# Kernel tuning notes

Hardware: AMD Instinct MI355X
Metric: run time of the kernel (lower is better)

Reference implementation:

```python
import jax, jax.numpy as jnp
import numpy as np

EPS = 1e-7
BETA = 1.0


def setup_inputs() -> dict:
    key = jax.random.key(0)
    k1, k2, k3, k4 = jax.random.split(key, 4)
    N, E, D_IN, D_OUT = 50000, 800000, 96, 96
    feat = jax.random.normal(k1, (N, D_IN), dtype=jnp.float32)
    src = jax.random.randint(k2, (E,), 0, N, dtype=jnp.int32)
    dst = jax.random.randint(k3, (E,), 0, N, dtype=jnp.int32)
    W = jax.random.normal(k4, (D_IN, D_OUT), dtype=jnp.float32) / np.sqrt(D_IN)
    b = jnp.zeros((D_OUT,), dtype=jnp.float32)
    return {"feat": feat, "src": src, "dst": dst, "W": W, "b": b}


def reference(feat, src, dst, W, b):
    # GENConv with softmax aggregation (canonical DeeperGCN semantics):
    # per edge e=(u,v): m_e = relu(h_u) + eps
    #                   a_e = softmax over edges into v of (beta * m_e)  (per feature dim)
    #                   msg_v = sum_e a_e * m_e
    # out = MLP(h + msg), MLP here = single Linear (mlp_layers=1)
    N = feat.shape[0]
    m = jax.nn.relu(feat[src]) + EPS                     # [E, D]
    logits = BETA * m                                    # [E, D]
    # numerically stable segment softmax over incoming edges of each dst node
    seg_max = jax.ops.segment_max(logits, dst, num_segments=N)   # [N, D]
    ex = jnp.exp(logits - seg_max[dst])                  # [E, D]
    denom = jax.ops.segment_sum(ex, dst, num_segments=N)         # [N, D]
    a = ex / denom[dst]                                  # [E, D]
    msg = jax.ops.segment_sum(a * m, dst, num_segments=N)        # [N, D]
    feats = feat + msg                                   # residual
    return feats @ W + b                                 # [N, D_out]
```

## Files before the change

### kernel.cpp

```cpp
#include <hip/hip_runtime.h>

#define D 96
#define EPSV 1e-7f
#define STRIDE 64
#define NB 16
#define TFUSED 192
#define EPB 2048
#define CAP 5120
#define HLP 100

__device__ __forceinline__ unsigned short f32_to_bf16_rtne(float x) {
    unsigned int u = __float_as_uint(x);
    u += 0x7fffu + ((u >> 16) & 1u);
    return (unsigned short)(u >> 16);
}
__device__ __forceinline__ float blo(uint u) { return __uint_as_float(u << 16); }
__device__ __forceinline__ float bhi(uint u) { return __uint_as_float(u & 0xFFFF0000u); }
__device__ __forceinline__ float bf16_to_f32(unsigned short u) {
    return __uint_as_float(((unsigned int)u) << 16);
}

__global__ __launch_bounds__(256) void part_conv(
    const int* __restrict__ src, const int* __restrict__ dst,
    uint* __restrict__ cursor,
    uint* __restrict__ stage,
    int E, int pblk,
    const float* __restrict__ feat, ushort* __restrict__ fb, int total4)
{
    __shared__ uint   hist[256];
    __shared__ uint   scn[256];
    __shared__ uint   xbase[256];
    __shared__ uint   gbase[256];
    __shared__ uint   sorted[EPB];
    __shared__ ushort sbid[EPB];

    int t = threadIdx.x;

    if ((int)blockIdx.x >= pblk) {
        int i = ((int)blockIdx.x - pblk) * 256 + t;
        if (i < total4) {
            const float4 f = reinterpret_cast<const float4*>(feat)[i];
            ushort4 o;
            o.x = f32_to_bf16_rtne(f.x);
            o.y = f32_to_bf16_rtne(f.y);
            o.z = f32_to_bf16_rtne(f.z);
            o.w = f32_to_bf16_rtne(f.w);
            reinterpret_cast<ushort4*>(fb)[i] = o;
        }
        return;
    }

    int e0 = blockIdx.x * EPB;
    int tot = E - e0; if (tot > EPB) tot = EPB;

    hist[t] = 0;
    __syncthreads();

    uint myb[EPB / 256], myrk[EPB / 256], myrec[EPB / 256];
    #pragma unroll
    for (int r = 0; r < EPB / 256; ++r) {
        int i = r * 256 + t;
        if (i < tot) {
            int d = dst[e0 + i];
            int s = src[e0 + i];
            uint b = (uint)d >> 8;
            myb[r]  = b;
            myrk[r] = atomicAdd(&hist[b], 1u);
            myrec[r] = (uint)(s & 0xFFFF) | ((uint)(d & 0xFF) << 16);
        }
    }
    __syncthreads();

    scn[t] = hist[t];
    __syncthreads();
    #pragma unroll
    for (int off = 1; off < 256; off <<= 1) {
        uint v = (t >= off) ? scn[t - off] : 0u;
        __syncthreads();
        scn[t] += v;
        __syncthreads();
    }
    xbase[t] = scn[t] - hist[t];
    if (hist[t] > 0)
        gbase[t] = (uint)t * CAP + atomicAdd(&cursor[t], hist[t]);
    __syncthreads();

    #pragma unroll
    for (int r = 0; r < EPB / 256; ++r) {
        int i = r * 256 + t;
        if (i < tot) {
            uint j = xbase[myb[r]] + myrk[r];
            sorted[j] = myrec[r];
            sbid[j]   = (ushort)myb[r];
        }
    }
    __syncthreads();

    #pragma unroll
    for (int r = 0; r < EPB / 256; ++r) {
        int j = r * 256 + t;
        if (j < tot) {
            uint b = sbid[j];
            uint gaddr = gbase[b] + ((uint)j - xbase[b]);
            if (gaddr - b * CAP < CAP)
                stage[gaddr] = sorted[j];
        }
    }
}

__global__ __launch_bounds__(256) void csr_build(
    const uint* __restrict__ cursor, const uint* __restrict__ stage,
    int* __restrict__ deg, ushort* __restrict__ csr, int N)
{
    __shared__ int ldeg[256];
    int b = blockIdx.x;
    int t = threadIdx.x;
    ldeg[t] = 0;
    __syncthreads();

    int cnt = (int)cursor[b]; if (cnt > CAP) cnt = CAP;
    const uint* sp = stage + (size_t)b * CAP;
    for (int i = t; i < cnt; i += 256) {
        uint rec = sp[i];
        int s  = rec & 0xFFFF;
        int dl = (rec >> 16) & 0xFF;
        int slot = atomicAdd(&ldeg[dl], 1);
        if (slot < STRIDE)
            csr[(size_t)((b << 8) + dl) * STRIDE + slot] = (ushort)s;
    }
    __syncthreads();
    int n = (b << 8) + t;
    if (n < N) deg[n] = min(ldeg[t], STRIDE);
}

__global__ __launch_bounds__(256) void build_fast(
    const float* __restrict__ feat, ushort* __restrict__ fb, int total4,
    const int* __restrict__ src, const int* __restrict__ dst,
    int* __restrict__ deg, ushort* __restrict__ csr, int E)
{
    int i = blockIdx.x * 256 + threadIdx.x;
    if (i < total4) {
        const float4 f = reinterpret_cast<const float4*>(feat)[i];
        ushort4 o;
        o.x = f32_to_bf16_rtne(f.x);
        o.y = f32_to_bf16_rtne(f.y);
        o.z = f32_to_bf16_rtne(f.z);
        o.w = f32_to_bf16_rtne(f.w);
        reinterpret_cast<ushort4*>(fb)[i] = o;
    } else {
        int e = i - total4;
        if (e < E) {
            int d = dst[e];
            int pos = atomicAdd(&deg[d], 1);
            if (pos < STRIDE) csr[(size_t)d * STRIDE + pos] = (ushort)src[e];
        }
    }
}

__global__ __launch_bounds__(TFUSED, 4) void fused_gather_gemm(
    const float* __restrict__ feat,
    const ushort* __restrict__ fb,
    const int* __restrict__ degp,
    const ushort* __restrict__ csr,
    const float* __restrict__ W,
    const float* __restrict__ bias,
    float* __restrict__ out,
    int N)
{
    __shared__ float  hl[NB][HLP];
    __shared__ ushort csr_l[NB * STRIDE];
    __shared__ int    degl[NB];

    int t = threadIdx.x;
    int nb0 = blockIdx.x * NB;

    {
        int nodes = N - nb0; if (nodes > NB) nodes = NB;
        int avail4 = (nodes * STRIDE) / 8;
        const uint4* gsrc = reinterpret_cast<const uint4*>(csr + (size_t)nb0 * STRIDE);
        uint4* ldst = reinterpret_cast<uint4*>(csr_l);
        if (t < avail4) ldst[t] = gsrc[t];
        if (t >= 128 && t < 128 + NB) {
            int nl = t - 128;
            int n = nb0 + nl;
            degl[nl] = (n < N) ? min(degp[n], STRIDE) : 0;
        }
    }
    __syncthreads();

    {
        int nl = t / 12;
        int q  = (t % 12) * 8;
        int n  = nb0 + nl;
        if (n < N) {
            int c = degl[nl];
            const ushort* cl = &csr_l[nl * STRIDE];

            float d0=0.f,d1=0.f,d2=0.f,d3=0.f,d4=0.f,d5=0.f,d6=0.f,d7=0.f;
            float a0=0.f,a1=0.f,a2=0.f,a3=0.f,a4=0.f,a5=0.f,a6=0.f,a7=0.f;

            #define PROC8(U) { \
                float m0 = fmaxf(blo((U).x), 0.f) + EPSV; \
                float m1 = fmaxf(bhi((U).x), 0.f) + EPSV; \
                float m2 = fmaxf(blo((U).y), 0.f) + EPSV; \
                float m3 = fmaxf(bhi((U).y), 0.f) + EPSV; \
                float m4 = fmaxf(blo((U).z), 0.f) + EPSV; \
                float m5 = fmaxf(bhi((U).z), 0.f) + EPSV; \
                float m6 = fmaxf(blo((U).w), 0.f) + EPSV; \
                float m7 = fmaxf(bhi((U).w), 0.f) + EPSV; \
                float e0=__expf(m0), e1=__expf(m1), e2=__expf(m2), e3=__expf(m3); \
                float e4=__expf(m4), e5=__expf(m5), e6=__expf(m6), e7=__expf(m7); \
                d0+=e0; d1+=e1; d2+=e2; d3+=e3; d4+=e4; d5+=e5; d6+=e6; d7+=e7; \
                a0=fmaf(e0,m0,a0); a1=fmaf(e1,m1,a1); a2=fmaf(e2,m2,a2); a3=fmaf(e3,m3,a3); \
                a4=fmaf(e4,m4,a4); a5=fmaf(e5,m5,a5); a6=fmaf(e6,m6,a6); a7=fmaf(e7,m7,a7); }

            int j = 0;
            for (; j + 4 <= c; j += 4) {
                const ushort4 ia = *reinterpret_cast<const ushort4*>(cl + j);
                const uint4 u0 = *reinterpret_cast<const uint4*>(fb + (size_t)ia.x * D + q);
                const uint4 u1 = *reinterpret_cast<const uint4*>(fb + (size_t)ia.y * D + q);
                const uint4 u2 = *reinterpret_cast<const uint4*>(fb + (size_t)ia.z * D + q);
                const uint4 u3 = *reinterpret_cast<const uint4*>(fb + (size_t)ia.w * D + q);
                PROC8(u0); PROC8(u1); PROC8(u2); PROC8(u3);
            }
            for (; j < c; ++j) {
                int s = cl[j];
                const uint4 u = *reinterpret_cast<const uint4*>(fb + (size_t)s * D + q);
                PROC8(u);
            }
            #undef PROC8

            const float4 bA = *reinterpret_cast<const float4*>(feat + (size_t)n * D + q);
            const float4 bB = *reinterpret_cast<const float4*>(feat + (size_t)n * D + q + 4);
            bool has = c > 0;
            float4 hA, hB;
            hA.x = bA.x + (has ? a0 / d0 : 0.f);
            hA.y = bA.y + (has ? a1 / d1 : 0.f);
            hA.z = bA.z + (has ? a2 / d2 : 0.f);
            hA.w = bA.w + (has ? a3 / d3 : 0.f);
            hB.x = bB.x + (has ? a4 / d4 : 0.f);
            hB.y = bB.y + (has ? a5 / d5 : 0.f);
            hB.z = bB.z + (has ? a6 / d6 : 0.f);
            hB.w = bB.w + (has ? a7 / d7 : 0.f);
            *reinterpret_cast<float4*>(&hl[nl][q])     = hA;
            *reinterpret_cast<float4*>(&hl[nl][q + 4]) = hB;
        }
    }
    __syncthreads();

    int q   = (t % 24) * 4;
    int grp = t / 24;
    int r0 = grp * 2, r1 = r0 + 1;
    float4 acc0 = *reinterpret_cast<const float4*>(bias + q);
    float4 acc1 = acc0;

    #pragma unroll 4
    for (int k = 0; k < D; ++k) {
        const float4 w = *reinterpret_cast<const float4*>(W + k * D + q);
        float h0 = hl[r0][k];
        float h1 = hl[r1][k];
        acc0.x = fmaf(h0, w.x, acc0.x); acc0.y = fmaf(h0, w.y, acc0.y);
        acc0.z = fmaf(h0, w.z, acc0.z); acc0.w = fmaf(h0, w.w, acc0.w);
        acc1.x = fmaf(h1, w.x, acc1.x); acc1.y = fmaf(h1, w.y, acc1.y);
        acc1.z = fmaf(h1, w.z, acc1.z); acc1.w = fmaf(h1, w.w, acc1.w);
    }

    int n0 = nb0 + r0;
    if (n0 + 0 < N) *reinterpret_cast<float4*>(out + (size_t)(n0 + 0) * D + q) = acc0;
    if (n0 + 1 < N) *reinterpret_cast<float4*>(out + (size_t)(n0 + 1) * D + q) = acc1;
}

extern "C" void kernel_launch(void* const* d_in, const int* in_sizes, int n_in,
                              void* d_out, int out_size, void* d_ws, size_t ws_size,
                              hipStream_t stream) {
    const float* feat = (const float*)d_in[0];
    const int*   src  = (const int*)d_in[1];
    const int*   dst  = (const int*)d_in[2];
    const float* W    = (const float*)d_in[3];
    const float* bias = (const float*)d_in[4];

    int N = in_sizes[0] / D;
    int E = in_sizes[1];
    int total4 = N * D / 4;
    int nbuck  = (N + 255) >> 8;

    size_t fb_bytes    = (size_t)N * D * sizeof(ushort);
    size_t deg_bytes   = (size_t)N * sizeof(int);
    size_t csr_bytes   = (size_t)N * STRIDE * sizeof(ushort);
    size_t cur_bytes   = 256 * sizeof(uint);
    size_t stage_bytes = (size_t)nbuck * CAP * sizeof(uint);

    size_t part_need  = fb_bytes + deg_bytes + csr_bytes + cur_bytes + stage_bytes;
    size_t fast_need  = fb_bytes + deg_bytes + csr_bytes;

    int gblocks = (N + NB - 1) / NB;

    ushort* fb  = (ushort*)d_ws;
    int*    deg = (int*)((char*)d_ws + fb_bytes);
    ushort* csr = (ushort*)((char*)deg + deg_bytes);

    if (ws_size >= part_need) {
        uint* cursor = (uint*)((char*)csr + csr_bytes);
        uint* stage  = (uint*)((char*)cursor + cur_bytes);

        int pblk = (E + EPB - 1) / EPB;
        int cblk = (total4 + 255) / 256;

        (void)hipMemsetAsync(cursor, 0, cur_bytes, stream);
        part_conv<<<pblk + cblk, 256, 0, stream>>>(
            src, dst, cursor, stage, E, pblk, feat, fb, total4);
        csr_build<<<nbuck, 256, 0, stream>>>(cursor, stage, deg, csr, N);
        fused_gather_gemm<<<gblocks, TFUSED, 0, stream>>>(
            feat, fb, deg, csr, W, bias, (float*)d_out, N);
    } else if (ws_size >= fast_need) {
        (void)hipMemsetAsync(deg, 0, deg_bytes, stream);
        int btotal = total4 + E;
        build_fast<<<(btotal + 255) / 256, 256, 0, stream>>>(
            feat, fb, total4, src, dst, deg, csr, E);
        fused_gather_gemm<<<gblocks, TFUSED, 0, stream>>>(
            feat, fb, deg, csr, W, bias, (float*)d_out, N);
    }
}
```

Before: 84.93 us.

## Scatter edges directly to global buckets and unroll gather loop by eight

The partition kernel no longer runs a block-wide prefix scan and local shared-memory sort before writing to the staging buckets. Each edge now goes straight to its global bucket slot, computed from the bucket base plus its atomic rank. This removes the scan's many syncs and the shared-memory traffic, but the global writes become less coalesced. Separately, the aggregation loop processes eight neighbor rows per iteration instead of four, putting more gathers in flight at the cost of more registers.

Result: slower. 92.01 us (+8.3%).

```diff
diff --git a/kernel.cpp b/kernel.cpp
--- a/kernel.cpp
+++ b/kernel.cpp
@@ -16,9 +16,6 @@
 }
 __device__ __forceinline__ float blo(uint u) { return __uint_as_float(u << 16); }
 __device__ __forceinline__ float bhi(uint u) { return __uint_as_float(u & 0xFFFF0000u); }
-__device__ __forceinline__ float bf16_to_f32(unsigned short u) {
-    return __uint_as_float(((unsigned int)u) << 16);
-}
 
 __global__ __launch_bounds__(256) void part_conv(
     const int* __restrict__ src, const int* __restrict__ dst,
@@ -27,12 +24,8 @@
     int E, int pblk,
     const float* __restrict__ feat, ushort* __restrict__ fb, int total4)
 {
-    __shared__ uint   hist[256];
-    __shared__ uint   scn[256];
-    __shared__ uint   xbase[256];
-    __shared__ uint   gbase[256];
-    __shared__ uint   sorted[EPB];
-    __shared__ ushort sbid[EPB];
+    __shared__ uint hist[256];
+    __shared__ uint gbase[256];
 
     int t = threadIdx.x;
 
@@ -71,16 +64,6 @@
     }
     __syncthreads();
 
-    scn[t] = hist[t];
-    __syncthreads();
-    #pragma unroll
-    for (int off = 1; off < 256; off <<= 1) {
-        uint v = (t >= off) ? scn[t - off] : 0u;
-        __syncthreads();
-        scn[t] += v;
-        __syncthreads();
-    }
-    xbase[t] = scn[t] - hist[t];
     if (hist[t] > 0)
         gbase[t] = (uint)t * CAP + atomicAdd(&cursor[t], hist[t]);
     __syncthreads();
@@ -89,21 +72,10 @@
     for (int r = 0; r < EPB / 256; ++r) {
         int i = r * 256 + t;
         if (i < tot) {
-            uint j = xbase[myb[r]] + myrk[r];
-            sorted[j] = myrec[r];
-            sbid[j]   = (ushort)myb[r];
-        }
-    }
-    __syncthreads();
-
-    #pragma unroll
-    for (int r = 0; r < EPB / 256; ++r) {
-        int j = r * 256 + t;
-        if (j < tot) {
-            uint b = sbid[j];
-            uint gaddr = gbase[b] + ((uint)j - xbase[b]);
+            uint b = myb[r];
+            uint gaddr = gbase[b] + myrk[r];
             if (gaddr - b * CAP < CAP)
-                stage[gaddr] = sorted[j];
+                stage[gaddr] = myrec[r];
         }
     }
 }
@@ -215,13 +187,28 @@
                 a4=fmaf(e4,m4,a4); a5=fmaf(e5,m5,a5); a6=fmaf(e6,m6,a6); a7=fmaf(e7,m7,a7); }
 
             int j = 0;
-            for (; j + 4 <= c; j += 4) {
+            for (; j + 8 <= c; j += 8) {
+                const ushort4 ia = *reinterpret_cast<const ushort4*>(cl + j);
+                const ushort4 ib = *reinterpret_cast<const ushort4*>(cl + j + 4);
+                const uint4 u0 = *reinterpret_cast<const uint4*>(fb + (size_t)ia.x * D + q);
+                const uint4 u1 = *reinterpret_cast<const uint4*>(fb + (size_t)ia.y * D + q);
+                const uint4 u2 = *reinterpret_cast<const uint4*>(fb + (size_t)ia.z * D + q);
+                const uint4 u3 = *reinterpret_cast<const uint4*>(fb + (size_t)ia.w * D + q);
+                const uint4 u4 = *reinterpret_cast<const uint4*>(fb + (size_t)ib.x * D + q);
+                const uint4 u5 = *reinterpret_cast<const uint4*>(fb + (size_t)ib.y * D + q);
+                const uint4 u6 = *reinterpret_cast<const uint4*>(fb + (size_t)ib.z * D + q);
+                const uint4 u7 = *reinterpret_cast<const uint4*>(fb + (size_t)ib.w * D + q);
+                PROC8(u0); PROC8(u1); PROC8(u2); PROC8(u3);
+                PROC8(u4); PROC8(u5); PROC8(u6); PROC8(u7);
+            }
+            if (j + 4 <= c) {
                 const ushort4 ia = *reinterpret_cast<const ushort4*>(cl + j);
                 const uint4 u0 = *reinterpret_cast<const uint4*>(fb + (size_t)ia.x * D + q);
                 const uint4 u1 = *reinterpret_cast<const uint4*>(fb + (size_t)ia.y * D + q);
                 const uint4 u2 = *reinterpret_cast<const uint4*>(fb + (size_t)ia.z * D + q);
                 const uint4 u3 = *reinterpret_cast<const uint4*>(fb + (size_t)ia.w * D + q);
                 PROC8(u0); PROC8(u1); PROC8(u2); PROC8(u3);
+                j += 4;
             }
             for (; j < c; ++j) {
                 int s = cl[j];
```
